# Kernel tuning notes

Hardware: AMD Instinct MI355X
Metric: run time of the kernel (lower is better)

The kernel has to match this reference:

```python
import jax, jax.numpy as jnp
import numpy as np

B, NV, HID, TDIM = 1024, 256, 256, 128
NODE_IN = 2 + 4 + TDIM  # coords + pos_enc(4) + time_emb


def _sinusoidal_pos_emb(t, dim):
    # standard SinusoidalPosEmb: cat(sin, cos) of t * exp(-i*log(1e4)/(half-1))
    half = dim // 2
    freqs = jnp.exp(-np.log(10000.0) * jnp.arange(half, dtype=t.dtype) / (half - 1))
    ang = t[:, None] * freqs[None, :]
    return jnp.concatenate([jnp.sin(ang), jnp.cos(ang)], axis=-1)  # [B, dim]


def setup_inputs() -> dict:
    key = jax.random.key(0)
    ks = jax.random.split(key, 10)
    s = lambda fan_in: 1.0 / np.sqrt(fan_in)
    return {
        "x": jax.random.normal(ks[0], (B, NV * 2), dtype=jnp.float32),
        "t": jax.random.uniform(ks[1], (B,), dtype=jnp.float32) * 1000.0,
        "time_w": jax.random.normal(ks[2], (TDIM, TDIM), dtype=jnp.float32) * s(TDIM),
        "time_b": jnp.zeros((TDIM,), dtype=jnp.float32),
        "W0": jax.random.normal(ks[3], (NODE_IN, HID), dtype=jnp.float32) * s(NODE_IN),
        "b0": jnp.zeros((HID,), dtype=jnp.float32),
        "W1": jax.random.normal(ks[4], (HID, HID), dtype=jnp.float32) * s(HID),
        "b1": jnp.zeros((HID,), dtype=jnp.float32),
        "W2": jax.random.normal(ks[5], (HID, HID), dtype=jnp.float32) * s(HID),
        "b2": jnp.zeros((HID,), dtype=jnp.float32),
    }


def reference(x, t, time_w, time_b, W0, b0, W1, b1, W2, b2):
    Bsz, D = x.shape
    n = D // 2
    coords = x.reshape(Bsz, n, 2)  # [B, n, 2]

    # cycle positional features (pos_enc_dim=4): sin/cos of vertex angle + 2nd harmonic
    pos = jnp.arange(n, dtype=x.dtype)
    theta = (2.0 * jnp.pi) * pos / n
    pe = jnp.stack([jnp.sin(theta), jnp.cos(theta), jnp.sin(2.0 * theta), jnp.cos(2.0 * theta)], axis=-1)
    pe = jnp.broadcast_to(pe[None], (Bsz, n, 4))

    # time MLP: SinusoidalPosEmb -> Linear -> SiLU, broadcast to every node of the graph
    temb = jax.nn.silu(_sinusoidal_pos_emb(t, time_w.shape[0]) @ time_w + time_b)  # [B, TDIM]
    temb = jnp.broadcast_to(temb[:, None, :], (Bsz, n, temb.shape[-1]))

    h = jnp.concatenate([coords, pe, temb], axis=-1)  # [B, n, NODE_IN]

    # GCN layers over cycle adjacency with self-loops, symmetric-normalized (deg=3 -> 1/3).
    # Cycle structure: neighbors are prev/next vertex within each polygon -> jnp.roll on axis 1.
    for W, b in ((W0, b0), (W1, b1), (W2, b2)):
        s = h @ W + b  # support = x W + b
        agg = (s + jnp.roll(s, 1, axis=1) + jnp.roll(s, -1, axis=1)) / 3.0
        h = jax.nn.silu(agg)

    # mean pooling per graph (scatter_mean over graph_index == mean over vertex axis here)
    return h.mean(axis=1)  # [B, HID]
```

## Files before the change

kernel.cpp:

```cpp
#include <hip/hip_runtime.h>
#include <cstdint>

typedef __attribute__((ext_vector_type(8)))  short bf16x8;
typedef __attribute__((ext_vector_type(16))) float f32x16;
typedef __attribute__((ext_vector_type(4)))  int   i32x4;

__device__ __forceinline__ unsigned short f2bf(float x) {
  unsigned u = __float_as_uint(x);
  u += 0x7fffu + ((u >> 16) & 1u);
  return (unsigned short)(u >> 16);
}
__device__ __forceinline__ float bf2f(unsigned short h) {
  return __uint_as_float(((unsigned)h) << 16);
}
__device__ __forceinline__ unsigned pk2bf(float lo, float hi) {
#if defined(__has_builtin)
#if __has_builtin(__builtin_amdgcn_cvt_pk_bf16_f32)
  auto v = __builtin_amdgcn_cvt_pk_bf16_f32(lo, hi);
  unsigned u; __builtin_memcpy(&u, &v, 4); return u;
#else
  return ((unsigned)f2bf(hi) << 16) | (unsigned)f2bf(lo);
#endif
#else
  return ((unsigned)f2bf(hi) << 16) | (unsigned)f2bf(lo);
#endif
}
__device__ __forceinline__ float silu_f(float v) {
  return v * __builtin_amdgcn_rcpf(1.0f + __expf(-v));
}
__device__ __forceinline__ unsigned lo_pack(unsigned x, unsigned y) {
  return __builtin_amdgcn_perm(y, x, 0x05040100u);
}
__device__ __forceinline__ unsigned hi_pack(unsigned x, unsigned y) {
  return __builtin_amdgcn_perm(y, x, 0x07060302u);
}

__global__ void pack_kernel(const float* __restrict__ W0, const float* __restrict__ W1,
                            const float* __restrict__ W2,
                            unsigned short* __restrict__ packW) {
  __shared__ float ldsF[16][257];
  const int s = blockIdx.x, tid = threadIdx.x;
  const float* W; int KT, kmax, base, kt;
  if (s < 9)       { W = W0; KT = 9;  kmax = 134; base = 0;      kt = s; }
  else if (s < 25) { W = W1; KT = 16; kmax = 256; base = 36864;  kt = s - 9; }
  else             { W = W2; KT = 16; kmax = 256; base = 102400; kt = s - 25; }
  const int k0 = kt * 16;
#pragma unroll
  for (int i = 0; i < 8; ++i) {
    const int idx = i * 512 + tid;
    const int kl = idx >> 8, col = idx & 255;
    const int kg = k0 + kl;
    ldsF[kl][col] = (kg < kmax) ? W[kg * 256 + col] : 0.0f;
  }
  __syncthreads();
  const int g = tid >> 7, t = (tid >> 6) & 1, lane = tid & 63;
  const int col = g * 64 + t * 32 + (lane & 31);
  const int kb = 8 * (lane >> 5);
  unsigned u0 = pk2bf(ldsF[kb + 0][col], ldsF[kb + 1][col]);
  unsigned u1 = pk2bf(ldsF[kb + 2][col], ldsF[kb + 3][col]);
  unsigned u2 = pk2bf(ldsF[kb + 4][col], ldsF[kb + 5][col]);
  unsigned u3 = pk2bf(ldsF[kb + 6][col], ldsF[kb + 7][col]);
  unsigned short* dst = packW + base + g * (KT * 1024) + t * (KT * 512) + kt * 512 + lane * 8;
  i32x4 v = { (int)u0, (int)u1, (int)u2, (int)u3 };
  *(i32x4*)dst = v;
}

struct EpiPre {
  float e0t0, e0t1, e15t0, e15t1, bp0, bp1, bn0, bn1, bias0, bias1;
};

template <int KT, int LAYER>
__device__ __forceinline__ void gcn_layer(
    const int w, const int lane, const int q, const int c, const int sig,
    const int wp, const int wn, const int ebase,
    const unsigned short* __restrict__ packL,
    const float* __restrict__ BIAS,
    const bf16x8* Aold, bf16x8* Anew,
    unsigned short* bndE, unsigned int* flagsL,
    unsigned int* scr3_w, float* poolw) {
  const float T = 0.33333333333f;
  f32x16 a0[2], a1[2];
  EpiPre ep;
  float ps0 = 0.f, ps1 = 0.f;

  auto spin = [&](int ww, int e) {
    while (__hip_atomic_load(&flagsL[e * 8 + ww], __ATOMIC_ACQUIRE,
                             __HIP_MEMORY_SCOPE_WORKGROUP) == 0u)
      __builtin_amdgcn_s_sleep(1);
  };
  auto publish = [&](int g, const f32x16& C0, const f32x16& C1) {
    unsigned short* myb = bndE + ((ebase + g) * 8 + w) * 128;
    if (q == 0) { myb[c]      = f2bf(C0[0]);  myb[32 + c] = f2bf(C1[0]);  }
    else        { myb[64 + c] = f2bf(C0[15]); myb[96 + c] = f2bf(C1[15]); }
    if (lane == 0)
      __hip_atomic_store(&flagsL[(ebase + g) * 8 + w], 1u, __ATOMIC_RELEASE,
                         __HIP_MEMORY_SCOPE_WORKGROUP);
  };
  auto epi_prep = [&](int pg, const f32x16& P0, const f32x16& P1) {
    const int e = ebase + pg;
    ep.e0t0  = __shfl_xor(P0[0], 32);  ep.e0t1  = __shfl_xor(P1[0], 32);
    ep.e15t0 = __shfl_xor(P0[15], 32); ep.e15t1 = __shfl_xor(P1[15], 32);
    ep.bp0 = bf2f(bndE[(e * 8 + wp) * 128 + 64 + c]);
    ep.bp1 = bf2f(bndE[(e * 8 + wp) * 128 + 96 + c]);
    ep.bn0 = bf2f(bndE[(e * 8 + wn) * 128 + c]);
    ep.bn1 = bf2f(bndE[(e * 8 + wn) * 128 + 32 + c]);
    ep.bias0 = BIAS[pg * 64 + c]; ep.bias1 = BIAS[pg * 64 + 32 + c];
    ps0 = 0.f; ps1 = 0.f;
  };
  auto epi_iter = [&](int r, const f32x16& P0, const f32x16& P1) {
    float pr0, pr1, nx0, nx1;
    if (r > 0)  { pr0 = P0[r - 1]; pr1 = P1[r - 1]; }
    else        { pr0 = q ? ep.e15t0 : ep.bp0; pr1 = q ? ep.e15t1 : ep.bp1; }
    if (r < 15) { nx0 = P0[r + 1]; nx1 = P1[r + 1]; }
    else        { nx0 = q ? ep.bn0 : ep.e0t0; nx1 = q ? ep.bn1 : ep.e0t1; }
    const float v0 = (pr0 + P0[r] + nx0) * T + ep.bias0;
    const float v1 = (pr1 + P1[r] + nx1) * T + ep.bias1;
    const float y0 = silu_f(v0);
    const float y1 = silu_f(v1);
    if constexpr (LAYER == 2) { ps0 += y0; ps1 += y1; }
    else scr3_w[(16 * q + r) * 34 + c] = pk2bf(y0, y1);
  };
  auto epi_fini = [&](int pg) {
    if constexpr (LAYER == 2) {
      float s0 = ps0 + __shfl_xor(ps0, 32);
      float s1 = ps1 + __shfl_xor(ps1, 32);
      if (q == 0) { poolw[w * 256 + pg * 64 + c]      = s0;
                    poolw[w * 256 + pg * 64 + 32 + c] = s1; }
    } else {
      const unsigned int* sb = scr3_w + sig * 34;
      uint2 d0 = *(const uint2*)(sb + 8 * q + 0);
      uint2 d1 = *(const uint2*)(sb + 8 * q + 2);
      uint2 d2 = *(const uint2*)(sb + 8 * q + 4);
      uint2 d3 = *(const uint2*)(sb + 8 * q + 6);
      uint2 e0 = *(const uint2*)(sb + 16 + 8 * q + 0);
      uint2 e1 = *(const uint2*)(sb + 16 + 8 * q + 2);
      uint2 e2 = *(const uint2*)(sb + 16 + 8 * q + 4);
      uint2 e3 = *(const uint2*)(sb + 16 + 8 * q + 6);
      i32x4 f0 = { (int)lo_pack(d0.x, d0.y), (int)lo_pack(d1.x, d1.y),
                   (int)lo_pack(d2.x, d2.y), (int)lo_pack(d3.x, d3.y) };
      i32x4 f1 = { (int)lo_pack(e0.x, e0.y), (int)lo_pack(e1.x, e1.y),
                   (int)lo_pack(e2.x, e2.y), (int)lo_pack(e3.x, e3.y) };
      i32x4 f2v = { (int)hi_pack(d0.x, d0.y), (int)hi_pack(d1.x, d1.y),
                    (int)hi_pack(d2.x, d2.y), (int)hi_pack(d3.x, d3.y) };
      i32x4 f3 = { (int)hi_pack(e0.x, e0.y), (int)hi_pack(e1.x, e1.y),
                   (int)hi_pack(e2.x, e2.y), (int)hi_pack(e3.x, e3.y) };
      Anew[pg * 4 + 0] = __builtin_bit_cast(bf16x8, f0);
      Anew[pg * 4 + 1] = __builtin_bit_cast(bf16x8, f1);
      Anew[pg * 4 + 2] = __builtin_bit_cast(bf16x8, f2v);
      Anew[pg * 4 + 3] = __builtin_bit_cast(bf16x8, f3);
    }
  };
  auto run_group = [&](int g, f32x16& C0, f32x16& C1,
                       const f32x16& P0, const f32x16& P1, bool doEpi) {
    const bf16x8* wb0 = (const bf16x8*)(packL + g * (KT * 1024));
    const bf16x8* wb1 = (const bf16x8*)(packL + g * (KT * 1024) + KT * 512);
#pragma unroll
    for (int i = 0; i < 16; ++i) { C0[i] = 0.f; C1[i] = 0.f; }
    bf16x8 pb0[2], pb1[2];
    pb0[0] = wb0[lane]; pb1[0] = wb1[lane];
    if (KT > 1) { pb0[1] = wb0[64 + lane]; pb1[1] = wb1[64 + lane]; }
#pragma unroll
    for (int kt = 0; kt < KT; ++kt) {
      bf16x8 b0 = pb0[kt & 1], b1 = pb1[kt & 1];
      if (kt + 2 < KT) { pb0[kt & 1] = wb0[(kt + 2) * 64 + lane];
                         pb1[kt & 1] = wb1[(kt + 2) * 64 + lane]; }
      C0 = __builtin_amdgcn_mfma_f32_32x32x16_bf16(Aold[kt], b0, C0, 0, 0, 0);
      C1 = __builtin_amdgcn_mfma_f32_32x32x16_bf16(Aold[kt], b1, C1, 0, 0, 0);
      if (doEpi) {
#pragma unroll
        for (int r = (kt * 16) / KT; r < ((kt + 1) * 16) / KT; ++r)
          epi_iter(r, P0, P1);
      }
    }
  };

  run_group(0, a0[0], a1[0], a0[0], a1[0], false);
  publish(0, a0[0], a1[0]);
#pragma unroll
  for (int g = 1; g <= 3; ++g) {
    const int pg = g - 1, pp = pg & 1, cp = g & 1;
    spin(wp, ebase + pg); spin(wn, ebase + pg);
    epi_prep(pg, a0[pp], a1[pp]);
    run_group(g, a0[cp], a1[cp], a0[pp], a1[pp], true);
    epi_fini(pg);
    publish(g, a0[cp], a1[cp]);
  }
  spin(wp, ebase + 3); spin(wn, ebase + 3);
  epi_prep(3, a0[1], a1[1]);
#pragma unroll
  for (int r = 0; r < 16; ++r) epi_iter(r, a0[1], a1[1]);
  epi_fini(3);
}

__global__ __launch_bounds__(512, 2) void poly_kernel(
    const float* __restrict__ x, const float* __restrict__ t,
    const float* __restrict__ tw, const float* __restrict__ tb,
    const unsigned short* __restrict__ packW,
    const float* __restrict__ B0, const float* __restrict__ B1,
    const float* __restrict__ B2, float* __restrict__ out) {
  __shared__ __align__(16) unsigned short bndE[12288];
  __shared__ unsigned int flagsL[96];
  __shared__ __align__(16) unsigned int   scr3[8 * 1088];
  __shared__ float poolL[2048];
  __shared__ __align__(16) unsigned short temb_sh[160];

  const int tid = threadIdx.x;
  const int w = tid >> 6, lane = tid & 63;
  const int q = lane >> 5, c = lane & 31;
  const int wp = (w + 7) & 7, wn = (w + 1) & 7;
  const int b = blockIdx.x;
  const int sig = (c & 3) + 4 * ((c >> 3) & 3) + 16 * ((c >> 2) & 1);

  if (lane < 12) flagsL[lane * 8 + w] = 0;

  {
    float* e_sh = (float*)bndE;
    float* part = (float*)scr3;
    if (tid < 128) {
      const float tv = t[b];
      const int i = tid & 63;
      const float f = expf(-0.14619588396823767f * (float)i);
      const float ang = tv * f;
      e_sh[tid] = (tid < 64) ? sinf(ang) : cosf(ang);
    }
    __syncthreads();
    {
      const int j = tid & 127, p = tid >> 7;
      float a = 0.f;
#pragma unroll 8
      for (int kk = 0; kk < 32; ++kk) {
        const int k = p * 32 + kk;
        a += e_sh[k] * tw[k * 128 + j];
      }
      part[tid] = a;
    }
    __syncthreads();
    if (tid < 128) {
      const float a = tb[tid] + part[tid] + part[128 + tid] + part[256 + tid] + part[384 + tid];
      temb_sh[6 + tid] = f2bf(silu_f(a));
      if (tid < 6)  temb_sh[tid] = 0;
      if (tid < 10) temb_sh[134 + tid] = 0;
    }
    __syncthreads();
  }

  bf16x8 A0[9], A1[16], A2[16];
  {
#pragma unroll
    for (int kt = 0; kt < 9; ++kt)
      A0[kt] = *(const bf16x8*)(temb_sh + kt * 16 + q * 8);
    if (q == 0) {
      const int n = w * 32 + sig;
      const float2 xy = ((const float2*)x)[b * 256 + n];
      const float th = 0.024543692605870074f * (float)n;
      A0[0][0] = (short)f2bf(xy.x);
      A0[0][1] = (short)f2bf(xy.y);
      A0[0][2] = (short)f2bf(sinf(th));
      A0[0][3] = (short)f2bf(cosf(th));
      A0[0][4] = (short)f2bf(sinf(2.f * th));
      A0[0][5] = (short)f2bf(cosf(2.f * th));
    }
  }

  unsigned int* scr3_w = scr3 + w * 1088;
  gcn_layer< 9, 0>(w, lane, q, c, sig, wp, wn, 0, packW,          B0, A0, A1,
                   bndE, flagsL, scr3_w, poolL);
  gcn_layer<16, 1>(w, lane, q, c, sig, wp, wn, 4, packW + 36864,  B1, A1, A2,
                   bndE, flagsL, scr3_w, poolL);
  gcn_layer<16, 2>(w, lane, q, c, sig, wp, wn, 8, packW + 102400, B2, A2, A1,
                   bndE, flagsL, scr3_w, poolL);

  __syncthreads();
  if (tid < 256) {
    float s = 0.f;
#pragma unroll
    for (int ww = 0; ww < 8; ++ww) s += poolL[ww * 256 + tid];
    out[b * 256 + tid] = s * (1.f / 256.f);
  }
}

extern "C" void kernel_launch(void* const* d_in, const int* in_sizes, int n_in,
                              void* d_out, int out_size, void* d_ws, size_t ws_size,
                              hipStream_t stream) {
  const float* x  = (const float*)d_in[0];
  const float* t  = (const float*)d_in[1];
  const float* tw = (const float*)d_in[2];
  const float* tb = (const float*)d_in[3];
  const float* W0 = (const float*)d_in[4];
  const float* b0 = (const float*)d_in[5];
  const float* W1 = (const float*)d_in[6];
  const float* b1 = (const float*)d_in[7];
  const float* W2 = (const float*)d_in[8];
  const float* b2 = (const float*)d_in[9];

  unsigned short* packW = (unsigned short*)d_ws;
  float* out = (float*)d_out;

  pack_kernel<<<41, 512, 0, stream>>>(W0, W1, W2, packW);
  poly_kernel<<<1024, 512, 0, stream>>>(x, t, tw, tb, packW, b0, b1, b2, out);
}
```

Before: 204.6 us.

## Swap GEMM roles so each wave owns output columns with weights held in registers

```diff
diff --git a/kernel.cpp b/kernel.cpp
--- a/kernel.cpp
+++ b/kernel.cpp
@@ -9,9 +9,6 @@
   unsigned u = __float_as_uint(x);
   u += 0x7fffu + ((u >> 16) & 1u);
   return (unsigned short)(u >> 16);
-}
-__device__ __forceinline__ float bf2f(unsigned short h) {
-  return __uint_as_float(((unsigned)h) << 16);
 }
 __device__ __forceinline__ unsigned pk2bf(float lo, float hi) {
 #if defined(__has_builtin)
@@ -28,12 +25,6 @@
 __device__ __forceinline__ float silu_f(float v) {
   return v * __builtin_amdgcn_rcpf(1.0f + __expf(-v));
 }
-__device__ __forceinline__ unsigned lo_pack(unsigned x, unsigned y) {
-  return __builtin_amdgcn_perm(y, x, 0x05040100u);
-}
-__device__ __forceinline__ unsigned hi_pack(unsigned x, unsigned y) {
-  return __builtin_amdgcn_perm(y, x, 0x07060302u);
-}
 
 __global__ void pack_kernel(const float* __restrict__ W0, const float* __restrict__ W1,
                             const float* __restrict__ W2,
@@ -65,131 +56,70 @@
   *(i32x4*)dst = v;
 }
 
-struct EpiPre {
-  float e0t0, e0t1, e15t0, e15t1, bp0, bp1, bn0, bn1, bias0, bias1;
-};
-
-template <int KT, int LAYER>
-__device__ __forceinline__ void gcn_layer(
-    const int w, const int lane, const int q, const int c, const int sig,
-    const int wp, const int wn, const int ebase,
-    const unsigned short* __restrict__ packL,
-    const float* __restrict__ BIAS,
-    const bf16x8* Aold, bf16x8* Anew,
-    unsigned short* bndE, unsigned int* flagsL,
-    unsigned int* scr3_w, float* poolw) {
+
+template <int KT>
+__device__ __forceinline__ void kloop(const unsigned short* __restrict__ hbuf,
+                                      const bf16x8* Bf, const int q, const int c,
+                                      f32x16* acc) {
+#pragma unroll
+  for (int nt = 0; nt < 8; ++nt)
+#pragma unroll
+    for (int j = 0; j < 16; ++j) acc[nt][j] = 0.f;
+#pragma unroll
+  for (int kt = 0; kt < KT; ++kt) {
+    const unsigned short* base = hbuf + c * 256 + (((2 * kt + q) ^ c) * 8);
+    bf16x8 Af[8];
+#pragma unroll
+    for (int nt = 0; nt < 8; ++nt)
+      Af[nt] = *(const bf16x8*)(base + nt * 8192);
+#pragma unroll
+    for (int nt = 0; nt < 8; ++nt)
+      acc[nt] = __builtin_amdgcn_mfma_f32_32x32x16_bf16(Af[nt], Bf[kt], acc[nt], 0, 0, 0);
+  }
+}
+
+template <int LAYER>
+__device__ __forceinline__ void epilogue(f32x16* acc, const int q, const float bias,
+                                         unsigned short* __restrict__ hbuf,
+                                         const int* rowAddr, float& psum) {
   const float T = 0.33333333333f;
-  f32x16 a0[2], a1[2];
-  EpiPre ep;
-  float ps0 = 0.f, ps1 = 0.f;
-
-  auto spin = [&](int ww, int e) {
-    while (__hip_atomic_load(&flagsL[e * 8 + ww], __ATOMIC_ACQUIRE,
-                             __HIP_MEMORY_SCOPE_WORKGROUP) == 0u)
-      __builtin_amdgcn_s_sleep(1);
-  };
-  auto publish = [&](int g, const f32x16& C0, const f32x16& C1) {
-    unsigned short* myb = bndE + ((ebase + g) * 8 + w) * 128;
-    if (q == 0) { myb[c]      = f2bf(C0[0]);  myb[32 + c] = f2bf(C1[0]);  }
-    else        { myb[64 + c] = f2bf(C0[15]); myb[96 + c] = f2bf(C1[15]); }
-    if (lane == 0)
-      __hip_atomic_store(&flagsL[(ebase + g) * 8 + w], 1u, __ATOMIC_RELEASE,
-                         __HIP_MEMORY_SCOPE_WORKGROUP);
-  };
-  auto epi_prep = [&](int pg, const f32x16& P0, const f32x16& P1) {
-    const int e = ebase + pg;
-    ep.e0t0  = __shfl_xor(P0[0], 32);  ep.e0t1  = __shfl_xor(P1[0], 32);
-    ep.e15t0 = __shfl_xor(P0[15], 32); ep.e15t1 = __shfl_xor(P1[15], 32);
-    ep.bp0 = bf2f(bndE[(e * 8 + wp) * 128 + 64 + c]);
-    ep.bp1 = bf2f(bndE[(e * 8 + wp) * 128 + 96 + c]);
-    ep.bn0 = bf2f(bndE[(e * 8 + wn) * 128 + c]);
-    ep.bn1 = bf2f(bndE[(e * 8 + wn) * 128 + 32 + c]);
-    ep.bias0 = BIAS[pg * 64 + c]; ep.bias1 = BIAS[pg * 64 + 32 + c];
-    ps0 = 0.f; ps1 = 0.f;
-  };
-  auto epi_iter = [&](int r, const f32x16& P0, const f32x16& P1) {
-    float pr0, pr1, nx0, nx1;
-    if (r > 0)  { pr0 = P0[r - 1]; pr1 = P1[r - 1]; }
-    else        { pr0 = q ? ep.e15t0 : ep.bp0; pr1 = q ? ep.e15t1 : ep.bp1; }
-    if (r < 15) { nx0 = P0[r + 1]; nx1 = P1[r + 1]; }
-    else        { nx0 = q ? ep.bn0 : ep.e0t0; nx1 = q ? ep.bn1 : ep.e0t1; }
-    const float v0 = (pr0 + P0[r] + nx0) * T + ep.bias0;
-    const float v1 = (pr1 + P1[r] + nx1) * T + ep.bias1;
-    const float y0 = silu_f(v0);
-    const float y1 = silu_f(v1);
-    if constexpr (LAYER == 2) { ps0 += y0; ps1 += y1; }
-    else scr3_w[(16 * q + r) * 34 + c] = pk2bf(y0, y1);
-  };
-  auto epi_fini = [&](int pg) {
-    if constexpr (LAYER == 2) {
-      float s0 = ps0 + __shfl_xor(ps0, 32);
-      float s1 = ps1 + __shfl_xor(ps1, 32);
-      if (q == 0) { poolw[w * 256 + pg * 64 + c]      = s0;
-                    poolw[w * 256 + pg * 64 + 32 + c] = s1; }
-    } else {
-      const unsigned int* sb = scr3_w + sig * 34;
-      uint2 d0 = *(const uint2*)(sb + 8 * q + 0);
-      uint2 d1 = *(const uint2*)(sb + 8 * q + 2);
-      uint2 d2 = *(const uint2*)(sb + 8 * q + 4);
-      uint2 d3 = *(const uint2*)(sb + 8 * q + 6);
-      uint2 e0 = *(const uint2*)(sb + 16 + 8 * q + 0);
-      uint2 e1 = *(const uint2*)(sb + 16 + 8 * q + 2);
-      uint2 e2 = *(const uint2*)(sb + 16 + 8 * q + 4);
-      uint2 e3 = *(const uint2*)(sb + 16 + 8 * q + 6);
-      i32x4 f0 = { (int)lo_pack(d0.x, d0.y), (int)lo_pack(d1.x, d1.y),
-                   (int)lo_pack(d2.x, d2.y), (int)lo_pack(d3.x, d3.y) };
-      i32x4 f1 = { (int)lo_pack(e0.x, e0.y), (int)lo_pack(e1.x, e1.y),
-                   (int)lo_pack(e2.x, e2.y), (int)lo_pack(e3.x, e3.y) };
-      i32x4 f2v = { (int)hi_pack(d0.x, d0.y), (int)hi_pack(d1.x, d1.y),
-                    (int)hi_pack(d2.x, d2.y), (int)hi_pack(d3.x, d3.y) };
-      i32x4 f3 = { (int)hi_pack(e0.x, e0.y), (int)hi_pack(e1.x, e1.y),
-                   (int)hi_pack(e2.x, e2.y), (int)hi_pack(e3.x, e3.y) };
-      Anew[pg * 4 + 0] = __builtin_bit_cast(bf16x8, f0);
-      Anew[pg * 4 + 1] = __builtin_bit_cast(bf16x8, f1);
-      Anew[pg * 4 + 2] = __builtin_bit_cast(bf16x8, f2v);
-      Anew[pg * 4 + 3] = __builtin_bit_cast(bf16x8, f3);
-    }
-  };
-  auto run_group = [&](int g, f32x16& C0, f32x16& C1,
-                       const f32x16& P0, const f32x16& P1, bool doEpi) {
-    const bf16x8* wb0 = (const bf16x8*)(packL + g * (KT * 1024));
-    const bf16x8* wb1 = (const bf16x8*)(packL + g * (KT * 1024) + KT * 512);
-#pragma unroll
-    for (int i = 0; i < 16; ++i) { C0[i] = 0.f; C1[i] = 0.f; }
-    bf16x8 pb0[2], pb1[2];
-    pb0[0] = wb0[lane]; pb1[0] = wb1[lane];
-    if (KT > 1) { pb0[1] = wb0[64 + lane]; pb1[1] = wb1[64 + lane]; }
-#pragma unroll
-    for (int kt = 0; kt < KT; ++kt) {
-      bf16x8 b0 = pb0[kt & 1], b1 = pb1[kt & 1];
-      if (kt + 2 < KT) { pb0[kt & 1] = wb0[(kt + 2) * 64 + lane];
-                         pb1[kt & 1] = wb1[(kt + 2) * 64 + lane]; }
-      C0 = __builtin_amdgcn_mfma_f32_32x32x16_bf16(Aold[kt], b0, C0, 0, 0, 0);
-      C1 = __builtin_amdgcn_mfma_f32_32x32x16_bf16(Aold[kt], b1, C1, 0, 0, 0);
-      if (doEpi) {
-#pragma unroll
-        for (int r = (kt * 16) / KT; r < ((kt + 1) * 16) / KT; ++r)
-          epi_iter(r, P0, P1);
+  float c7[8];
+#pragma unroll
+  for (int nt = 0; nt < 8; ++nt) {
+    const float send = q ? acc[nt][15] : acc[(nt + 1) & 7][0];
+    c7[nt] = __shfl_xor(send, 32);
+  }
+#pragma unroll
+  for (int nt = 0; nt < 8; ++nt) {
+    float rk[7];
+#pragma unroll
+    for (int k = 0; k < 7; ++k) {
+      const int lowReg = 4 * (k >> 1) + 3;
+      const int upReg  = 4 * ((k + 1) >> 1);
+      const float send = (q == (k & 1)) ? acc[nt][lowReg] : acc[nt][upReg];
+      rk[k] = __shfl_xor(send, 32);
+    }
+#pragma unroll
+    for (int r = 0; r < 16; ++r) {
+      float prev, next;
+      if ((r & 3) > 0) prev = acc[nt][r - 1];
+      else {
+        const float pq1 = rk[2 * (r >> 2)];
+        const float pq0 = (r == 0) ? c7[(nt + 7) & 7] : rk[2 * (r >> 2) - 1];
+        prev = q ? pq1 : pq0;
       }
-    }
-  };
-
-  run_group(0, a0[0], a1[0], a0[0], a1[0], false);
-  publish(0, a0[0], a1[0]);
-#pragma unroll
-  for (int g = 1; g <= 3; ++g) {
-    const int pg = g - 1, pp = pg & 1, cp = g & 1;
-    spin(wp, ebase + pg); spin(wn, ebase + pg);
-    epi_prep(pg, a0[pp], a1[pp]);
-    run_group(g, a0[cp], a1[cp], a0[pp], a1[pp], true);
-    epi_fini(pg);
-    publish(g, a0[cp], a1[cp]);
-  }
-  spin(wp, ebase + 3); spin(wn, ebase + 3);
-  epi_prep(3, a0[1], a1[1]);
-#pragma unroll
-  for (int r = 0; r < 16; ++r) epi_iter(r, a0[1], a1[1]);
-  epi_fini(3);
+      if ((r & 3) < 3) next = acc[nt][r + 1];
+      else {
+        const float nq0 = rk[2 * (r >> 2)];
+        const float nq1 = (r == 15) ? c7[nt] : rk[2 * (r >> 2) + 1];
+        next = q ? nq1 : nq0;
+      }
+      const float v = (prev + acc[nt][r] + next) * T + bias;
+      const float y = silu_f(v);
+      if constexpr (LAYER == 2) psum += y;
+      else *(unsigned short*)((char*)hbuf + nt * 16384 + rowAddr[r]) = f2bf(y);
+    }
+  }
 }
 
 __global__ __launch_bounds__(512, 2) void poly_kernel(
@@ -198,85 +128,94 @@
     const unsigned short* __restrict__ packW,
     const float* __restrict__ B0, const float* __restrict__ B1,
     const float* __restrict__ B2, float* __restrict__ out) {
-  __shared__ __align__(16) unsigned short bndE[12288];
-  __shared__ unsigned int flagsL[96];
-  __shared__ __align__(16) unsigned int   scr3[8 * 1088];
-  __shared__ float poolL[2048];
-  __shared__ __align__(16) unsigned short temb_sh[160];
+  __shared__ __align__(16) unsigned short hbuf[65536];
+  __shared__ __align__(16) unsigned short tmpl[160];
 
   const int tid = threadIdx.x;
-  const int w = tid >> 6, lane = tid & 63;
-  const int q = lane >> 5, c = lane & 31;
-  const int wp = (w + 7) & 7, wn = (w + 1) & 7;
+  const int w = tid >> 6, lane = tid & 63, q = lane >> 5, c = lane & 31;
   const int b = blockIdx.x;
-  const int sig = (c & 3) + 4 * ((c >> 3) & 3) + 16 * ((c >> 2) & 1);
-
-  if (lane < 12) flagsL[lane * 8 + w] = 0;
 
   {
-    float* e_sh = (float*)bndE;
-    float* part = (float*)scr3;
+    float* scr = (float*)hbuf;
     if (tid < 128) {
       const float tv = t[b];
       const int i = tid & 63;
       const float f = expf(-0.14619588396823767f * (float)i);
       const float ang = tv * f;
-      e_sh[tid] = (tid < 64) ? sinf(ang) : cosf(ang);
+      scr[tid] = (tid < 64) ? sinf(ang) : cosf(ang);
     }
     __syncthreads();
     {
       const int j = tid & 127, p = tid >> 7;
       float a = 0.f;
 #pragma unroll 8
-      for (int kk = 0; kk < 32; ++kk) {
-        const int k = p * 32 + kk;
-        a += e_sh[k] * tw[k * 128 + j];
-      }
-      part[tid] = a;
+      for (int kk = 0; kk < 32; ++kk) a += scr[p * 32 + kk] * tw[(p * 32 + kk) * 128 + j];
+      scr[128 + tid] = a;
     }
     __syncthreads();
     if (tid < 128) {
-      const float a = tb[tid] + part[tid] + part[128 + tid] + part[256 + tid] + part[384 + tid];
-      temb_sh[6 + tid] = f2bf(silu_f(a));
-      if (tid < 6)  temb_sh[tid] = 0;
-      if (tid < 10) temb_sh[134 + tid] = 0;
+      const float a = tb[tid] + scr[128 + tid] + scr[256 + tid] + scr[384 + tid] + scr[512 + tid];
+      tmpl[6 + tid] = f2bf(silu_f(a));
+      if (tid < 6)  tmpl[tid] = 0;
+      if (tid < 26) tmpl[134 + tid] = 0;
     }
     __syncthreads();
   }
 
-  bf16x8 A0[9], A1[16], A2[16];
-  {
-#pragma unroll
-    for (int kt = 0; kt < 9; ++kt)
-      A0[kt] = *(const bf16x8*)(temb_sh + kt * 16 + q * 8);
-    if (q == 0) {
-      const int n = w * 32 + sig;
-      const float2 xy = ((const float2*)x)[b * 256 + n];
-      const float th = 0.024543692605870074f * (float)n;
-      A0[0][0] = (short)f2bf(xy.x);
-      A0[0][1] = (short)f2bf(xy.y);
-      A0[0][2] = (short)f2bf(sinf(th));
-      A0[0][3] = (short)f2bf(cosf(th));
-      A0[0][4] = (short)f2bf(sinf(2.f * th));
-      A0[0][5] = (short)f2bf(cosf(2.f * th));
-    }
-  }
-
-  unsigned int* scr3_w = scr3 + w * 1088;
-  gcn_layer< 9, 0>(w, lane, q, c, sig, wp, wn, 0, packW,          B0, A0, A1,
-                   bndE, flagsL, scr3_w, poolL);
-  gcn_layer<16, 1>(w, lane, q, c, sig, wp, wn, 4, packW + 36864,  B1, A1, A2,
-                   bndE, flagsL, scr3_w, poolL);
-  gcn_layer<16, 2>(w, lane, q, c, sig, wp, wn, 8, packW + 102400, B2, A2, A1,
-                   bndE, flagsL, scr3_w, poolL);
-
-  __syncthreads();
-  if (tid < 256) {
-    float s = 0.f;
-#pragma unroll
-    for (int ww = 0; ww < 8; ++ww) s += poolL[ww * 256 + tid];
-    out[b * 256 + tid] = s * (1.f / 256.f);
-  }
+#pragma unroll
+  for (int i = 0; i < 9; ++i) {
+    const int task = tid + i * 512;
+    const int node = task & 255, slot = task >> 8;
+    i32x4 d = *(const i32x4*)(tmpl + slot * 8);
+    if (slot == 0) {
+      const float2 xy = ((const float2*)x)[b * 256 + node];
+      const float th = 0.024543692605870074f * (float)node;
+      d.x = (int)pk2bf(xy.x, xy.y);
+      d.y = (int)pk2bf(sinf(th), cosf(th));
+      d.z = (int)pk2bf(sinf(2.f * th), cosf(2.f * th));
+    }
+    *(i32x4*)(hbuf + node * 256 + ((slot ^ (node & 31)) * 8)) = d;
+  }
+
+  int rowAddr[16];
+  const int slotW = 4 * w + (c >> 3), offW = (c & 7) * 2;
+#pragma unroll
+  for (int r = 0; r < 16; ++r) {
+    const int row = (r & 3) + 8 * (r >> 2) + 4 * q;
+    rowAddr[r] = row * 512 + ((slotW ^ row) * 16) + offW;
+  }
+
+  const unsigned short* pL0 = packW + (w >> 1) * (9 * 1024) + (w & 1) * (9 * 512);
+  const unsigned short* pL1 = packW + 36864 + (w >> 1) * (16 * 1024) + (w & 1) * (16 * 512);
+  const unsigned short* pL2 = packW + 102400 + (w >> 1) * (16 * 1024) + (w & 1) * (16 * 512);
+  bf16x8 Bf[16];
+#pragma unroll
+  for (int kt = 0; kt < 9; ++kt) Bf[kt] = *(const bf16x8*)(pL0 + kt * 512 + lane * 8);
+  const float bias0 = B0[w * 32 + c], bias1 = B1[w * 32 + c], bias2 = B2[w * 32 + c];
+  __syncthreads();
+
+  f32x16 acc[8];
+  float psum = 0.f;
+
+  kloop<9>(hbuf, Bf, q, c, acc);
+  __syncthreads();
+#pragma unroll
+  for (int kt = 0; kt < 16; ++kt) Bf[kt] = *(const bf16x8*)(pL1 + kt * 512 + lane * 8);
+  epilogue<0>(acc, q, bias0, hbuf, rowAddr, psum);
+  __syncthreads();
+
+  kloop<16>(hbuf, Bf, q, c, acc);
+  __syncthreads();
+#pragma unroll
+  for (int kt = 0; kt < 16; ++kt) Bf[kt] = *(const bf16x8*)(pL2 + kt * 512 + lane * 8);
+  epilogue<1>(acc, q, bias1, hbuf, rowAddr, psum);
+  __syncthreads();
+
+  kloop<16>(hbuf, Bf, q, c, acc);
+  epilogue<2>(acc, q, bias2, hbuf, rowAddr, psum);
+
+  const float s2 = psum + __shfl_xor(psum, 32);
+  if (q == 0) out[b * 256 + w * 32 + c] = s2 * (1.0f / 256.0f);
 }
 
 extern "C" void kernel_launch(void* const* d_in, const int* in_sizes, int n_in,
```

Result: slower. 711.0 us (+247.5%).
